# Kernel optimization log

Measured on AMD Instinct MI355X. Metric: run time of the kernel, lower is better.

Reference implementation:

```python
import jax, jax.numpy as jnp
import numpy as np

OUT, IN = 14336, 4096          # Llama FFN up-projection
N = OUT * IN                   # total quantized elements
NB = N // 64                   # NF4 blocks (blocksize 64)
NG = N // 256                  # double-quant groups (group size 256)
B = 32                         # batch rows


def setup_inputs() -> dict:
    key = jax.random.key(0)
    ks = jax.random.split(key, 7)
    x = jax.random.normal(ks[0], (B, IN), dtype=jnp.float16)
    # packed bytes: two 4-bit nibbles per byte (values 0..255)
    packed = jax.random.randint(ks[1], (N // 2,), 0, 256, dtype=jnp.int32)
    absmax = jax.random.uniform(ks[2], (NB,), dtype=jnp.float32)                     # per-block absmax
    code = jax.random.uniform(ks[3], (NB,), jnp.float32, minval=0.5, maxval=1.5)     # per-block code scale
    offset = jax.random.uniform(ks[4], (NB,), jnp.float32, minval=0.0, maxval=8.0)   # per-block offset
    g_absmax = jax.random.uniform(ks[5], (NG,), jnp.float32, minval=0.5, maxval=1.5) # nested (state2) absmax
    g_code = jax.random.uniform(ks[6], (NG,), jnp.float32, minval=0.5, maxval=1.5)   # nested (state2) code
    return {"x": x, "packed": packed, "absmax": absmax, "code": code,
            "offset": offset, "g_absmax": g_absmax, "g_code": g_code}


def _dequantize_nf4(packed, absmax, code, offset, g_absmax, g_code):
    # Unpack nibbles: even element = low nibble (byte & 15), odd = high nibble (byte >> 4)
    low = packed & 15
    high = packed >> 4
    nib = jnp.stack([low, high], axis=-1).reshape(-1).astype(jnp.float32)  # [N]
    # Nested (double) dequantization scales, matching the Triton kernel:
    # combined_scale = (absmax / code) * (g_absmax / g_code)
    block_scale = absmax / code                      # [NB]
    group_scale = g_absmax / g_code                  # [NG]
    cs_block = block_scale * jnp.repeat(group_scale, 64 * 4 // 64)  # each group spans 4 blocks -> [NB]
    cs = jnp.repeat(cs_block, 64)                    # per-element combined scale [N]
    off = jnp.repeat(offset, 64)                     # per-element offset [N]
    # dequantized = nibble * cs - offset * cs (as written in the kernel), stored as fp16
    deq = (nib * cs - off * cs).astype(jnp.float16)
    return deq.reshape(OUT, IN)


def reference(x, packed, absmax, code, offset, g_absmax, g_code):
    W = _dequantize_nf4(packed, absmax, code, offset, g_absmax, g_code)  # [OUT, IN] fp16
    return x @ W.T                                                        # [B, OUT] fp16
```

## Files before the change

kernel.cpp:

```cpp
#include <hip/hip_runtime.h>
#include <hip/hip_bf16.h>


#define OUT_D 14336
#define IN_D  4096
#define B_D   32
#define KC    256
#define OTILE 32
#define NCHUNK (IN_D / KC)
#define LSTRIDE 264

typedef __attribute__((ext_vector_type(4))) float f32x4;
typedef __bf16 bf16x8 __attribute__((ext_vector_type(8)));
typedef __bf16 bf16x4 __attribute__((ext_vector_type(4)));
using u16 = unsigned short;

__global__ __launch_bounds__(256) void nf4_linear_kernel(
    const float* __restrict__ x,
    const int*  __restrict__ packed,
    const float* __restrict__ absmax,
    const float* __restrict__ code,
    const float* __restrict__ offset,
    const float* __restrict__ g_absmax,
    const float* __restrict__ g_code,
    float* __restrict__ out)
{
    __shared__ u16 wlds[OTILE * LSTRIDE];
    __shared__ u16 xlds[B_D * LSTRIDE];

    const int t      = threadIdx.x;
    const int o_base = blockIdx.x * OTILE;

    const int wrow = t >> 3;
    const int wseg = t & 7;
    const int o    = o_base + wrow;

    const int wave   = t >> 6;
    const int lane   = t & 63;
    const int m_base = (wave & 1) * 16;
    const int n_base = (wave >> 1) * 16;
    const int frow   = lane & 15;
    const int kk     = (lane >> 4) * 8;

    f32x4 acc = {0.f, 0.f, 0.f, 0.f};

    for (int kc = 0; kc < NCHUNK; ++kc) {
        #pragma unroll
        for (int j = 0; j < 8; ++j) {
            int li = t + j * 256;
            int xr = li >> 6;
            int xc = (li & 63) * 4;
            f32x4 v = *reinterpret_cast<const f32x4*>(x + xr * IN_D + kc * KC + xc);
            bf16x4 h;
            h[0] = (__bf16)v[0]; h[1] = (__bf16)v[1];
            h[2] = (__bf16)v[2]; h[3] = (__bf16)v[3];
            *reinterpret_cast<bf16x4*>(&xlds[xr * LSTRIDE + xc]) = h;
        }

        const int bidx = o * 64 + kc * 4 + (wseg >> 1);
        const int gidx = o * 16 + kc;
        const float cs  = (absmax[bidx] / code[bidx]) * (g_absmax[gidx] / g_code[gidx]);
        const float noc = -offset[bidx] * cs;

        const int* psrc = packed + o * (IN_D / 2) + kc * (KC / 2) + wseg * 16;
        #pragma unroll
        for (int j = 0; j < 4; ++j) {
            bf16x8 r;
            #pragma unroll
            for (int wi = 0; wi < 4; ++wi) {
                int w = psrc[j * 4 + wi];
                float lo = (float)(w & 15);
                float hi = (float)((w >> 4) & 15);
                r[wi * 2]     = (__bf16)fmaf(lo, cs, noc);
                r[wi * 2 + 1] = (__bf16)fmaf(hi, cs, noc);
            }
            *reinterpret_cast<bf16x8*>(&wlds[wrow * LSTRIDE + wseg * 32 + j * 8]) = r;
        }
        __syncthreads();

        const u16* xrow_p = &xlds[(m_base + frow) * LSTRIDE + kk];
        const u16* wrow_p = &wlds[(n_base + frow) * LSTRIDE + kk];
        #pragma unroll
        for (int ks = 0; ks < KC / 32; ++ks) {
            bf16x8 a = *reinterpret_cast<const bf16x8*>(xrow_p + ks * 32);
            bf16x8 b = *reinterpret_cast<const bf16x8*>(wrow_p + ks * 32);
            acc = __builtin_amdgcn_mfma_f32_16x16x32_bf16(a, b, acc, 0, 0, 0);
        }
        __syncthreads();
    }

    const int oc = o_base + n_base + frow;
    const int r0 = m_base + (lane >> 4) * 4;
    #pragma unroll
    for (int i = 0; i < 4; ++i) {
        out[(r0 + i) * OUT_D + oc] = acc[i];
    }
}

extern "C" void kernel_launch(void* const* d_in, const int* in_sizes, int n_in,
                              void* d_out, int out_size, void* d_ws, size_t ws_size,
                              hipStream_t stream) {
    const void* px = nullptr;
    const void* ppk = nullptr;
    const void* trio[3] = {nullptr, nullptr, nullptr};
    const void* pair[2] = {nullptr, nullptr};
    int ntrio = 0, npair = 0;
    const int SZ_X   = B_D * IN_D;
    const int SZ_PK  = OUT_D * (IN_D / 2);
    const int SZ_NB  = OUT_D * (IN_D / 64);
    const int SZ_NG  = OUT_D * (IN_D / 256);
    for (int i = 0; i < n_in; ++i) {
        int s = in_sizes[i];
        if (s == SZ_X) px = d_in[i];
        else if (s == SZ_PK) ppk = d_in[i];
        else if (s == SZ_NB) { if (ntrio < 3) trio[ntrio++] = d_in[i]; }
        else if (s == SZ_NG) { if (npair < 2) pair[npair++] = d_in[i]; }
    }
    if (!px || !ppk || ntrio != 3 || npair != 2) {
        px = d_in[0]; ppk = d_in[1];
        trio[0] = d_in[2]; trio[1] = d_in[3]; trio[2] = d_in[4];
        pair[0] = d_in[5]; pair[1] = d_in[6];
    }

    nf4_linear_kernel<<<dim3(OUT_D / OTILE), dim3(256), 0, stream>>>(
        (const float*)px, (const int*)ppk,
        (const float*)trio[0], (const float*)trio[1], (const float*)trio[2],
        (const float*)pair[0], (const float*)pair[1],
        (float*)d_out);
}
```

Before: 41.19 us.

## Dequantize weights directly into MFMA registers with split-K and prefetch pipeline

```diff
diff --git a/kernel.cpp b/kernel.cpp
--- a/kernel.cpp
+++ b/kernel.cpp
@@ -5,18 +5,25 @@
 #define OUT_D 14336
 #define IN_D  4096
 #define B_D   32
-#define KC    256
-#define OTILE 32
-#define NCHUNK (IN_D / KC)
-#define LSTRIDE 264
 
 typedef __attribute__((ext_vector_type(4))) float f32x4;
+typedef __attribute__((ext_vector_type(4))) int   i32x4;
 typedef __bf16 bf16x8 __attribute__((ext_vector_type(8)));
 typedef __bf16 bf16x4 __attribute__((ext_vector_type(4)));
 using u16 = unsigned short;
 
-__global__ __launch_bounds__(256) void nf4_linear_kernel(
-    const float* __restrict__ x,
+__global__ __launch_bounds__(256) void xconv_kernel(const float* __restrict__ x,
+                                                    u16* __restrict__ xb) {
+    int i = (blockIdx.x * 256 + threadIdx.x) * 4;
+    f32x4 v = *reinterpret_cast<const f32x4*>(x + i);
+    bf16x4 h;
+    h[0] = (__bf16)v[0]; h[1] = (__bf16)v[1];
+    h[2] = (__bf16)v[2]; h[3] = (__bf16)v[3];
+    *reinterpret_cast<bf16x4*>(xb + i) = h;
+}
+
+__global__ __launch_bounds__(256) void nf4_kernel(
+    const u16*  __restrict__ xb,
     const int*  __restrict__ packed,
     const float* __restrict__ absmax,
     const float* __restrict__ code,
@@ -25,76 +32,73 @@
     const float* __restrict__ g_code,
     float* __restrict__ out)
 {
-    __shared__ u16 wlds[OTILE * LSTRIDE];
-    __shared__ u16 xlds[B_D * LSTRIDE];
+    const int lane = threadIdx.x & 63;
+    const int wave = threadIdx.x >> 6;
+    const int frow = lane & 15;
+    const int fk   = lane >> 4;
+    const int o    = blockIdx.x * 64 + wave * 16 + frow;
+    const int kz   = blockIdx.y;
 
-    const int t      = threadIdx.x;
-    const int o_base = blockIdx.x * OTILE;
+    const int* wp  = packed + o * (IN_D / 2) + kz * (IN_D / 4) + fk * 4;
+    const u16* xlo = xb + frow * IN_D + kz * (IN_D / 2) + fk * 8;
+    const u16* xhi = xlo + 16 * IN_D;
+    const int  sb  = o * 64 + kz * 32;
+    const int  gb  = o * 16 + kz * 8;
 
-    const int wrow = t >> 3;
-    const int wseg = t & 7;
-    const int o    = o_base + wrow;
+    f32x4 acc0 = {0.f, 0.f, 0.f, 0.f};
+    f32x4 acc1 = {0.f, 0.f, 0.f, 0.f};
 
-    const int wave   = t >> 6;
-    const int lane   = t & 63;
-    const int m_base = (wave & 1) * 16;
-    const int n_base = (wave >> 1) * 16;
-    const int frow   = lane & 15;
-    const int kk     = (lane >> 4) * 8;
+    i32x4  w0, w1, w2, w3;
+    bf16x8 xl0, xl1, xl2, xl3;
+    bf16x8 xh0, xh1, xh2, xh3;
+    float cs0, noc0, cs1, noc1, csn0, nocn0, csn1, nocn1;
 
-    f32x4 acc = {0.f, 0.f, 0.f, 0.f};
+#define ISSUE(J, S) \
+    w##J  = *reinterpret_cast<const i32x4*>(wp + (S) * 16); \
+    xl##J = *reinterpret_cast<const bf16x8*>(xlo + (S) * 32); \
+    xh##J = *reinterpret_cast<const bf16x8*>(xhi + (S) * 32);
 
-    for (int kc = 0; kc < NCHUNK; ++kc) {
-        #pragma unroll
-        for (int j = 0; j < 8; ++j) {
-            int li = t + j * 256;
-            int xr = li >> 6;
-            int xc = (li & 63) * 4;
-            f32x4 v = *reinterpret_cast<const f32x4*>(x + xr * IN_D + kc * KC + xc);
-            bf16x4 h;
-            h[0] = (__bf16)v[0]; h[1] = (__bf16)v[1];
-            h[2] = (__bf16)v[2]; h[3] = (__bf16)v[3];
-            *reinterpret_cast<bf16x4*>(&xlds[xr * LSTRIDE + xc]) = h;
-        }
+#define LOADSC(CS, NOC, BLK) { \
+    float am = absmax[sb + (BLK)], cd = code[sb + (BLK)], of = offset[sb + (BLK)]; \
+    float ga = g_absmax[gb + ((BLK) >> 2)], gc = g_code[gb + ((BLK) >> 2)]; \
+    CS = (am * ga) / (cd * gc); NOC = -of * CS; }
 
-        const int bidx = o * 64 + kc * 4 + (wseg >> 1);
-        const int gidx = o * 16 + kc;
-        const float cs  = (absmax[bidx] / code[bidx]) * (g_absmax[gidx] / g_code[gidx]);
-        const float noc = -offset[bidx] * cs;
+#define PHASE(J, CS, NOC) { \
+    bf16x8 bf; \
+    _Pragma("unroll") \
+    for (int q = 0; q < 4; ++q) { \
+        int w = w##J[q]; \
+        bf[2 * q]     = (__bf16)fmaf((float)(w & 15),        CS, NOC); \
+        bf[2 * q + 1] = (__bf16)fmaf((float)((w >> 4) & 15), CS, NOC); \
+    } \
+    acc0 = __builtin_amdgcn_mfma_f32_16x16x32_bf16(xl##J, bf, acc0, 0, 0, 0); \
+    acc1 = __builtin_amdgcn_mfma_f32_16x16x32_bf16(xh##J, bf, acc1, 0, 0, 0); }
 
-        const int* psrc = packed + o * (IN_D / 2) + kc * (KC / 2) + wseg * 16;
-        #pragma unroll
-        for (int j = 0; j < 4; ++j) {
-            bf16x8 r;
-            #pragma unroll
-            for (int wi = 0; wi < 4; ++wi) {
-                int w = psrc[j * 4 + wi];
-                float lo = (float)(w & 15);
-                float hi = (float)((w >> 4) & 15);
-                r[wi * 2]     = (__bf16)fmaf(lo, cs, noc);
-                r[wi * 2 + 1] = (__bf16)fmaf(hi, cs, noc);
-            }
-            *reinterpret_cast<bf16x8*>(&wlds[wrow * LSTRIDE + wseg * 32 + j * 8]) = r;
-        }
-        __syncthreads();
+    ISSUE(0, 0) ISSUE(1, 1) ISSUE(2, 2) ISSUE(3, 3)
+    LOADSC(cs0, noc0, 0) LOADSC(cs1, noc1, 1)
 
-        const u16* xrow_p = &xlds[(m_base + frow) * LSTRIDE + kk];
-        const u16* wrow_p = &wlds[(n_base + frow) * LSTRIDE + kk];
-        #pragma unroll
-        for (int ks = 0; ks < KC / 32; ++ks) {
-            bf16x8 a = *reinterpret_cast<const bf16x8*>(xrow_p + ks * 32);
-            bf16x8 b = *reinterpret_cast<const bf16x8*>(wrow_p + ks * 32);
-            acc = __builtin_amdgcn_mfma_f32_16x16x32_bf16(a, b, acc, 0, 0, 0);
-        }
-        __syncthreads();
+    for (int g = 0; g < 15; ++g) {
+        const int s4 = g * 4 + 4;
+        LOADSC(csn0, nocn0, 2 * g + 2)
+        LOADSC(csn1, nocn1, 2 * g + 3)
+        PHASE(0, cs0, noc0)  ISSUE(0, s4 + 0)
+        PHASE(1, cs0, noc0)  ISSUE(1, s4 + 1)
+        PHASE(2, cs1, noc1)  ISSUE(2, s4 + 2)
+        PHASE(3, cs1, noc1)  ISSUE(3, s4 + 3)
+        cs0 = csn0; noc0 = nocn0; cs1 = csn1; noc1 = nocn1;
     }
+    PHASE(0, cs0, noc0) PHASE(1, cs0, noc0)
+    PHASE(2, cs1, noc1) PHASE(3, cs1, noc1)
 
-    const int oc = o_base + n_base + frow;
-    const int r0 = m_base + (lane >> 4) * 4;
+    const int r0 = fk * 4;
     #pragma unroll
     for (int i = 0; i < 4; ++i) {
-        out[(r0 + i) * OUT_D + oc] = acc[i];
+        atomicAdd(&out[(r0 + i) * OUT_D + o],      acc0[i]);
+        atomicAdd(&out[(r0 + 16 + i) * OUT_D + o], acc1[i]);
     }
+#undef ISSUE
+#undef LOADSC
+#undef PHASE
 }
 
 extern "C" void kernel_launch(void* const* d_in, const int* in_sizes, int n_in,
@@ -122,8 +126,14 @@
         pair[0] = d_in[5]; pair[1] = d_in[6];
     }
 
-    nf4_linear_kernel<<<dim3(OUT_D / OTILE), dim3(256), 0, stream>>>(
-        (const float*)px, (const int*)ppk,
+    u16* xbf = (u16*)d_ws;
+
+    xconv_kernel<<<dim3(SZ_X / 1024), dim3(256), 0, stream>>>((const float*)px, xbf);
+
+    hipMemsetAsync(d_out, 0, (size_t)out_size * sizeof(float), stream);
+
+    nf4_kernel<<<dim3(OUT_D / 64, 2), dim3(256), 0, stream>>>(
+        xbf, (const int*)ppk,
         (const float*)trio[0], (const float*)trio[1], (const float*)trio[2],
         (const float*)pair[0], (const float*)pair[1],
         (float*)d_out);
```

Measured after the change: 80.57 us. 95.6% more time.

## Split-K NF4 GEMV with precomputed scales, async LDS weight pipeline, and reduction

Applied to the files above, without the earlier changes.

```diff
diff --git a/kernel.cpp b/kernel.cpp
--- a/kernel.cpp
+++ b/kernel.cpp
@@ -5,96 +5,143 @@
 #define OUT_D 14336
 #define IN_D  4096
 #define B_D   32
-#define KC    256
-#define OTILE 32
-#define NCHUNK (IN_D / KC)
-#define LSTRIDE 264
+#define KSPLIT 8
+#define KRANGE (IN_D / KSPLIT)
+#define KC 64
+#define CHUNKS (KRANGE / KC)
+#define NB (OUT_D * IN_D / 64)
+#define SZ_X (B_D * IN_D)
 
 typedef __attribute__((ext_vector_type(4))) float f32x4;
+typedef __attribute__((ext_vector_type(2))) float f32x2;
+typedef __attribute__((ext_vector_type(4))) int   i32x4;
 typedef __bf16 bf16x8 __attribute__((ext_vector_type(8)));
-typedef __bf16 bf16x4 __attribute__((ext_vector_type(4)));
 using u16 = unsigned short;
 
-__global__ __launch_bounds__(256) void nf4_linear_kernel(
+typedef const __attribute__((address_space(1))) void* gas1_t;
+typedef __attribute__((address_space(3))) void* las3_t;
+
+__device__ __forceinline__ void gll16(const void* g, void* l) {
+    __builtin_amdgcn_global_load_lds((gas1_t)g, (las3_t)l, 16, 0, 0);
+}
+
+__global__ __launch_bounds__(256) void pre_kernel(
     const float* __restrict__ x,
-    const int*  __restrict__ packed,
-    const float* __restrict__ absmax,
-    const float* __restrict__ code,
+    const float* __restrict__ absmax, const float* __restrict__ code,
     const float* __restrict__ offset,
-    const float* __restrict__ g_absmax,
-    const float* __restrict__ g_code,
-    float* __restrict__ out)
+    const float* __restrict__ g_absmax, const float* __restrict__ g_code,
+    u16* __restrict__ xb, f32x2* __restrict__ csn)
 {
-    __shared__ u16 wlds[OTILE * LSTRIDE];
-    __shared__ u16 xlds[B_D * LSTRIDE];
+    const int i = blockIdx.x * 256 + threadIdx.x;
+    float am = absmax[i], cd = code[i], of = offset[i];
+    float ga = g_absmax[i >> 2], gc = g_code[i >> 2];
+    float cs = (am * ga) / (cd * gc);
+    f32x2 v; v.x = cs; v.y = -of * cs;
+    csn[i] = v;
+    if (i < SZ_X) {
+        __bf16 h = (__bf16)x[i];
+        xb[i] = __builtin_bit_cast(u16, h);
+    }
+}
+
+__global__ __launch_bounds__(256, 3) void nf4_main(
+    const u16* __restrict__ xb,
+    const int* __restrict__ packed,
+    const f32x2* __restrict__ csn,
+    float* __restrict__ part)
+{
+    __shared__ u16 xs[B_D][512];
+    __shared__ int wb[3][32][32];
 
     const int t      = threadIdx.x;
-    const int o_base = blockIdx.x * OTILE;
+    const int o_base = blockIdx.x * 32;
+    const int kz     = blockIdx.y;
 
-    const int wrow = t >> 3;
-    const int wseg = t & 7;
-    const int o    = o_base + wrow;
+    const int wave = t >> 6, lane = t & 63;
+    const int m_base = (wave & 1) * 16, n_base = (wave >> 1) * 16;
+    const int frow = lane & 15, q = lane >> 4;
+    const int rown = n_base + frow;
+    const int rowa = m_base + frow;
 
-    const int wave   = t >> 6;
-    const int lane   = t & 63;
-    const int m_base = (wave & 1) * 16;
-    const int n_base = (wave >> 1) * 16;
-    const int frow   = lane & 15;
-    const int kk     = (lane >> 4) * 8;
+    #pragma unroll
+    for (int j = 0; j < 8; ++j) {
+        int slot = t + j * 256;
+        int r = slot >> 6, c = slot & 63;
+        bf16x8 v = *reinterpret_cast<const bf16x8*>(xb + r * IN_D + kz * KRANGE + c * 8);
+        *reinterpret_cast<bf16x8*>(&xs[r][(c ^ (r & 7)) * 8]) = v;
+    }
+
+    f32x4 scp[4];
+    {
+        const f32x4* sp = reinterpret_cast<const f32x4*>(
+            csn + (o_base + rown) * 64 + kz * CHUNKS);
+        scp[0] = sp[0]; scp[1] = sp[1]; scp[2] = sp[2]; scp[3] = sp[3];
+    }
+    __builtin_amdgcn_sched_barrier(0);
+
+    const int srow = t >> 3;
+    const int scol = (t & 7) ^ (srow & 7);
+    const int* gsrc = packed + (o_base + srow) * (IN_D / 2)
+                             + kz * (KRANGE / 2) + scol * 4;
+
+    gll16(gsrc + 0 * 32, &wb[0][wave * 8][0]);
+    gll16(gsrc + 1 * 32, &wb[1][wave * 8][0]);
 
     f32x4 acc = {0.f, 0.f, 0.f, 0.f};
 
-    for (int kc = 0; kc < NCHUNK; ++kc) {
+    #pragma unroll
+    for (int C = 0; C < CHUNKS; ++C) {
+        if (C == 0)               asm volatile("s_waitcnt vmcnt(1) lgkmcnt(0)" ::: "memory");
+        else if (C < CHUNKS - 1)  asm volatile("s_waitcnt vmcnt(1)" ::: "memory");
+        else                      asm volatile("s_waitcnt vmcnt(0)" ::: "memory");
+        __builtin_amdgcn_s_barrier();
+        __builtin_amdgcn_sched_barrier(0);
+
+        if (C + 2 < CHUNKS)
+            gll16(gsrc + (C + 2) * 32, &wb[(C + 2) % 3][wave * 8][0]);
+
+        const int buf = C % 3;
+        const float cs  = scp[C >> 1][(C & 1) * 2];
+        const float noc = scp[C >> 1][(C & 1) * 2 + 1];
+
         #pragma unroll
-        for (int j = 0; j < 8; ++j) {
-            int li = t + j * 256;
-            int xr = li >> 6;
-            int xc = (li & 63) * 4;
-            f32x4 v = *reinterpret_cast<const f32x4*>(x + xr * IN_D + kc * KC + xc);
-            bf16x4 h;
-            h[0] = (__bf16)v[0]; h[1] = (__bf16)v[1];
-            h[2] = (__bf16)v[2]; h[3] = (__bf16)v[3];
-            *reinterpret_cast<bf16x4*>(&xlds[xr * LSTRIDE + xc]) = h;
-        }
-
-        const int bidx = o * 64 + kc * 4 + (wseg >> 1);
-        const int gidx = o * 16 + kc;
-        const float cs  = (absmax[bidx] / code[bidx]) * (g_absmax[gidx] / g_code[gidx]);
-        const float noc = -offset[bidx] * cs;
-
-        const int* psrc = packed + o * (IN_D / 2) + kc * (KC / 2) + wseg * 16;
-        #pragma unroll
-        for (int j = 0; j < 4; ++j) {
-            bf16x8 r;
+        for (int s = 0; s < 2; ++s) {
+            i32x4 braw = *reinterpret_cast<const i32x4*>(
+                &wb[buf][rown][(((s * 4 + q) ^ (rown & 7)) * 4)]);
+            int ca = C * 8 + s * 4 + q;
+            bf16x8 a = *reinterpret_cast<const bf16x8*>(
+                &xs[rowa][(ca ^ (rowa & 7)) * 8]);
+            bf16x8 b;
             #pragma unroll
-            for (int wi = 0; wi < 4; ++wi) {
-                int w = psrc[j * 4 + wi];
-                float lo = (float)(w & 15);
-                float hi = (float)((w >> 4) & 15);
-                r[wi * 2]     = (__bf16)fmaf(lo, cs, noc);
-                r[wi * 2 + 1] = (__bf16)fmaf(hi, cs, noc);
+            for (int w = 0; w < 4; ++w) {
+                int ww = braw[w];
+                b[2 * w]     = (__bf16)fmaf((float)(ww & 15),        cs, noc);
+                b[2 * w + 1] = (__bf16)fmaf((float)((ww >> 4) & 15), cs, noc);
             }
-            *reinterpret_cast<bf16x8*>(&wlds[wrow * LSTRIDE + wseg * 32 + j * 8]) = r;
-        }
-        __syncthreads();
-
-        const u16* xrow_p = &xlds[(m_base + frow) * LSTRIDE + kk];
-        const u16* wrow_p = &wlds[(n_base + frow) * LSTRIDE + kk];
-        #pragma unroll
-        for (int ks = 0; ks < KC / 32; ++ks) {
-            bf16x8 a = *reinterpret_cast<const bf16x8*>(xrow_p + ks * 32);
-            bf16x8 b = *reinterpret_cast<const bf16x8*>(wrow_p + ks * 32);
             acc = __builtin_amdgcn_mfma_f32_16x16x32_bf16(a, b, acc, 0, 0, 0);
         }
-        __syncthreads();
     }
 
+    float* pp = part + (size_t)kz * (B_D * OUT_D);
     const int oc = o_base + n_base + frow;
-    const int r0 = m_base + (lane >> 4) * 4;
+    const int r0 = m_base + q * 4;
     #pragma unroll
-    for (int i = 0; i < 4; ++i) {
-        out[(r0 + i) * OUT_D + oc] = acc[i];
+    for (int i = 0; i < 4; ++i)
+        pp[(r0 + i) * OUT_D + oc] = acc[i];
+}
+
+__global__ __launch_bounds__(256) void reduce_kernel(
+    const float* __restrict__ part, float* __restrict__ out)
+{
+    const int i = (blockIdx.x * 256 + threadIdx.x) * 4;
+    f32x4 s = *reinterpret_cast<const f32x4*>(part + i);
+    #pragma unroll
+    for (int k = 1; k < KSPLIT; ++k) {
+        f32x4 v = *reinterpret_cast<const f32x4*>(
+            part + (size_t)k * (B_D * OUT_D) + i);
+        s[0] += v[0]; s[1] += v[1]; s[2] += v[2]; s[3] += v[3];
     }
+    *reinterpret_cast<f32x4*>(out + i) = s;
 }
 
 extern "C" void kernel_launch(void* const* d_in, const int* in_sizes, int n_in,
@@ -105,9 +152,8 @@
     const void* trio[3] = {nullptr, nullptr, nullptr};
     const void* pair[2] = {nullptr, nullptr};
     int ntrio = 0, npair = 0;
-    const int SZ_X   = B_D * IN_D;
     const int SZ_PK  = OUT_D * (IN_D / 2);
-    const int SZ_NB  = OUT_D * (IN_D / 64);
+    const int SZ_NB  = NB;
     const int SZ_NG  = OUT_D * (IN_D / 256);
     for (int i = 0; i < n_in; ++i) {
         int s = in_sizes[i];
@@ -122,9 +168,20 @@
         pair[0] = d_in[5]; pair[1] = d_in[6];
     }
 
-    nf4_linear_kernel<<<dim3(OUT_D / OTILE), dim3(256), 0, stream>>>(
-        (const float*)px, (const int*)ppk,
+    char* ws = (char*)d_ws;
+    u16*   xb   = (u16*)ws;
+    f32x2* csn  = (f32x2*)(ws + 262144);
+    float* part = (float*)(ws + 262144 + (size_t)NB * 8);
+
+    pre_kernel<<<dim3(NB / 256), dim3(256), 0, stream>>>(
+        (const float*)px,
         (const float*)trio[0], (const float*)trio[1], (const float*)trio[2],
         (const float*)pair[0], (const float*)pair[1],
-        (float*)d_out);
+        xb, csn);
+
+    nf4_main<<<dim3(OUT_D / 32, KSPLIT), dim3(256), 0, stream>>>(
+        xb, (const int*)ppk, csn, part);
+
+    reduce_kernel<<<dim3(B_D * OUT_D / 4 / 256), dim3(256), 0, stream>>>(
+        part, (float*)d_out);
 }
```

Result: slower. 47.91 us (+16.3%).
